# Performance work log

Hardware: AMD Instinct MI355X
Metric: run time of the kernel (lower is better)

Reference implementation:

```python
import jax, jax.numpy as jnp
import numpy as np

N_NODES, N_EDGES, N_TRIP = 100000, 200000, 600000
HID, HEADS, RADIUS = 256, 8, 3
ATOM_F, BOND_F = 133, 14

def setup_inputs() -> dict:
    key = jax.random.key(0)
    ks = jax.random.split(key, 20)
    def w(k, i, o):
        return jax.random.normal(k, (i, o), dtype=jnp.float32) / np.sqrt(i)
    L = RADIUS - 1
    return {
        'atom_feature': jax.random.normal(ks[0], (N_NODES, ATOM_F), dtype=jnp.float32),
        'edge_feature': jax.random.normal(ks[1], (N_EDGES, BOND_F), dtype=jnp.float32),
        'W_i': w(ks[2], ATOM_F + BOND_F, HID),
        'Wq': jnp.stack([w(jax.random.fold_in(ks[3], l), HID, HID) for l in range(L)]),
        'Wk': jnp.stack([w(jax.random.fold_in(ks[4], l), HID, HID) for l in range(L)]),
        'Wv': jnp.stack([w(jax.random.fold_in(ks[5], l), HID, HID) for l in range(L)]),
        'L1w': jnp.stack([w(jax.random.fold_in(ks[6], l), HID, HID) for l in range(L)]),
        'L1b': jnp.zeros((L, HID), dtype=jnp.float32),
        'L2w': jnp.stack([w(jax.random.fold_in(ks[7], l), HID, HID) for l in range(L)]),
        'L2b': jnp.zeros((L, HID), dtype=jnp.float32),
        'Wo': w(ks[8], ATOM_F + HID, HID),
        'bo': jnp.zeros((HID,), dtype=jnp.float32),
        'src': jax.random.randint(ks[9], (N_EDGES,), 0, N_NODES, dtype=jnp.int32),
        'dst': jax.random.randint(ks[10], (N_EDGES,), 0, N_NODES, dtype=jnp.int32),
        'idx_kj': jax.random.randint(ks[11], (N_TRIP,), 0, N_EDGES, dtype=jnp.int32),
        'idx_ji': jax.random.randint(ks[12], (N_TRIP,), 0, N_EDGES, dtype=jnp.int32),
    }

def _att_layer(feats, Wq, Wk, Wv, l1w, l1b, l2w, l2b, idx_kj, idx_ji):
    E = feats.shape[0]
    d = HID // HEADS
    q = (feats @ Wq).reshape(E, HEADS, d)
    k = (feats @ Wk).reshape(E, HEADS, d)
    v = (feats @ Wv).reshape(E, HEADS, d)
    # per-triplet attention logits [T, heads, 1]
    att = jnp.sum(q[idx_kj] * k[idx_ji], axis=-1, keepdims=True)
    att = jnp.exp(jax.nn.leaky_relu(att, negative_slope=0.2))
    denom = jax.ops.segment_sum(att, idx_ji, num_segments=E)  # edge softmax norm
    att = att / denom[idx_ji]
    v_att = (v[idx_kj] * att).reshape(-1, HID)
    v_flat = v.reshape(E, HID)
    # v_clone = v + index_add(v_att) - v == segment_sum of messages
    v_clone = jax.ops.segment_sum(v_att, idx_ji, num_segments=E)
    # residual MLP (dropout p=0 -> identity)
    h = jax.nn.relu(jax.nn.relu(v_clone @ l1w + l1b) @ l2w + l2b)
    return v_flat + h

def reference(atom_feature, edge_feature, W_i, Wq, Wk, Wv, L1w, L1b, L2w, L2b, Wo, bo, src, dst, idx_kj, idx_ji):
    # per-edge initial feature: concat(src atom feature, edge feature)
    init = jnp.concatenate([atom_feature[src], edge_feature], axis=1)
    feats = jax.nn.relu(init @ W_i)
    for l in range(RADIUS - 1):
        feats = _att_layer(feats, Wq[l], Wk[l], Wv[l], L1w[l], L1b[l], L2w[l], L2b[l], idx_kj, idx_ji)
    # edge -> node sum (dgl update_all copy_e + sum onto dst)
    feats_sum = jax.ops.segment_sum(feats, dst, num_segments=atom_feature.shape[0])
    a_input = jnp.concatenate([atom_feature, feats_sum], axis=1)
    return jax.nn.relu(a_input @ Wo + bo)
```

## Files before the change

kernel.cpp:

```cpp
#include <hip/hip_runtime.h>
#include <stdint.h>

#define NN 100000
#define NNP 100096
#define NE 200000
#define NEP 200064
#define NT 600000
#define HID 256

typedef __attribute__((ext_vector_type(8))) short bf16x8;
typedef __attribute__((ext_vector_type(4))) float f32x4;

__device__ __forceinline__ float bf2f(unsigned short u) {
    union { unsigned int i; float f; } x; x.i = ((unsigned int)u) << 16; return x.f;
}
__device__ __forceinline__ unsigned short f2bf(float f) {
    union { float f; unsigned int i; } x; x.f = f;
    unsigned int r = (x.i + 0x7FFFu + ((x.i >> 16) & 1u)) >> 16;
    return (unsigned short)r;
}

__device__ __forceinline__ void gload16(const void* g, void* l) {
    __builtin_amdgcn_global_load_lds(
        (const __attribute__((address_space(1))) void*)g,
        (__attribute__((address_space(3))) void*)l, 16, 0, 0);
}

template<int FLAGS, bool CBF>
__device__ __forceinline__
void gemm128_core(const unsigned short* __restrict__ A,
                  const unsigned short* __restrict__ BT,
                  const float* __restrict__ bias,
                  const unsigned short* __restrict__ res,
                  void* __restrict__ Cv, int row0, int col0,
                  int Mreal, int Kpad,
                  unsigned short* Asb, unsigned short* Bsb)
{
    const int t    = threadIdx.x;
    const int lane = t & 63;
    const int wv   = t >> 6;
    const int wr   = wv >> 1;
    const int wc   = wv & 1;
    const int l15  = lane & 15;
    const int lk   = lane >> 4;
    const int sub  = lane >> 3;
    const int schk = lane & 7;

    f32x4 acc[4][4];
#pragma unroll
    for (int i = 0; i < 4; ++i)
#pragma unroll
        for (int j = 0; j < 4; ++j) acc[i][j] = (f32x4){0.f, 0.f, 0.f, 0.f};

    const int nt = Kpad >> 6;
    for (int kt = 0; kt < nt; ++kt) {
        const int k0 = kt << 6;
#pragma unroll
        for (int j = 0; j < 4; ++j) {
            const int ii = wv * 4 + j;
            const int r  = ii * 8 + sub;
            const int cg = schk ^ (r & 7);
            gload16(A + (size_t)(row0 + r) * Kpad + k0 + cg * 8, Asb + ii * 512);
        }
#pragma unroll
        for (int j = 0; j < 4; ++j) {
            const int ii = wv * 4 + j;
            const int r  = ii * 8 + sub;
            const int cg = schk ^ (r & 7);
            gload16(BT + (size_t)(col0 + r) * Kpad + k0 + cg * 8, Bsb + ii * 512);
        }
        __syncthreads();
#pragma unroll
        for (int ks = 0; ks < 2; ++ks) {
            bf16x8 af[4], bfg[4];
#pragma unroll
            for (int mi = 0; mi < 4; ++mi) {
                const int r = wr * 64 + mi * 16 + l15;
                const int c = ks * 4 + lk;
                af[mi] = *(const bf16x8*)((const char*)Asb
                          + r * 128 + ((c ^ (r & 7)) << 4));
            }
#pragma unroll
            for (int ni = 0; ni < 4; ++ni) {
                const int r = wc * 64 + ni * 16 + l15;
                const int c = ks * 4 + lk;
                bfg[ni] = *(const bf16x8*)((const char*)Bsb
                           + r * 128 + ((c ^ (r & 7)) << 4));
            }
#pragma unroll
            for (int mi = 0; mi < 4; ++mi)
#pragma unroll
                for (int ni = 0; ni < 4; ++ni)
                    acc[mi][ni] = __builtin_amdgcn_mfma_f32_16x16x32_bf16(
                        af[mi], bfg[ni], acc[mi][ni], 0, 0, 0);
        }
        __syncthreads();
    }

#pragma unroll
    for (int mi = 0; mi < 4; ++mi) {
#pragma unroll
        for (int r = 0; r < 4; ++r) {
            const int row = row0 + wr * 64 + mi * 16 + lk * 4 + r;
            if (row >= Mreal) continue;
#pragma unroll
            for (int ni = 0; ni < 4; ++ni) {
                const int col = col0 + wc * 64 + ni * 16 + l15;
                float o = acc[mi][ni][r];
                if (FLAGS & 2) o += bias[col];
                if (FLAGS & 1) o = fmaxf(o, 0.f);
                if (FLAGS & 4) o += bf2f(res[(size_t)row * HID + col]);
                if (CBF) ((unsigned short*)Cv)[(size_t)row * HID + col] = f2bf(o);
                else     ((float*)Cv)[(size_t)row * HID + col] = o;
            }
        }
    }
}

template<int FLAGS, bool CBF>
__global__ __launch_bounds__(256, 4)
void gemm128(const unsigned short* __restrict__ A,
             const unsigned short* __restrict__ BT,
             const float* __restrict__ bias,
             const unsigned short* __restrict__ res,
             void* __restrict__ Cv, int Mtiles, int Mreal, int Kpad)
{
    __shared__ alignas(16) unsigned short Asb[128 * 64];
    __shared__ alignas(16) unsigned short Bsb[128 * 64];
    const int x   = blockIdx.x;
    const int xcd = x & 7;
    const int ii  = x >> 3;
    const int g   = (ii >> 1) * 8 + xcd;
    const int ch  = ii & 1;
    if (g >= Mtiles) return;
    gemm128_core<FLAGS, CBF>(A, BT, bias, res, Cv, g * 128, ch * 128,
                             Mreal, Kpad, Asb, Bsb);
}

__global__ __launch_bounds__(256, 4)
void gemm128_qkv(const unsigned short* __restrict__ A,
                 const unsigned short* __restrict__ BTq,
                 const unsigned short* __restrict__ BTk,
                 const unsigned short* __restrict__ BTv,
                 unsigned short* __restrict__ Cq,
                 unsigned short* __restrict__ Ck,
                 unsigned short* __restrict__ Cvp, int Mtiles)
{
    __shared__ alignas(16) unsigned short Asb[128 * 64];
    __shared__ alignas(16) unsigned short Bsb[128 * 64];
    const int x   = blockIdx.x;
    const int xcd = x & 7;
    const int ii  = x >> 3;
    const int g   = (ii / 6) * 8 + xcd;
    const int j   = ii % 6;
    if (g >= Mtiles) return;
    const int proj = j >> 1;
    const int ch   = j & 1;
    const unsigned short* BT = (proj == 0) ? BTq : (proj == 1) ? BTk : BTv;
    unsigned short*       C  = (proj == 0) ? Cq  : (proj == 1) ? Ck  : Cvp;
    gemm128_core<0, true>(A, BT, nullptr, nullptr, C, g * 128, ch * 128,
                          NE, 256, Asb, Bsb);
}

__global__ __launch_bounds__(256)
void wconv(const float* __restrict__ W, unsigned short* __restrict__ BT,
           int Kreal, int Kpad)
{
    const int idx = blockIdx.x * 256 + threadIdx.x;
    const int n = idx / Kpad, kp = idx - n * Kpad;
    float v = (kp < Kreal) ? W[(size_t)kp * HID + n] : 0.f;
    BT[idx] = f2bf(v);
}

__global__ __launch_bounds__(256)
void wconv10(const float* __restrict__ Wq, const float* __restrict__ Wk,
             const float* __restrict__ Wv, const float* __restrict__ L1w,
             const float* __restrict__ L2w, unsigned short* __restrict__ outbase)
{
    const int y = blockIdx.y;
    const int l = y / 5, which = y - l * 5;
    const float* src;
    switch (which) {
        case 0: src = Wq;  break;
        case 1: src = Wk;  break;
        case 2: src = Wv;  break;
        case 3: src = L1w; break;
        default: src = L2w; break;
    }
    src += (size_t)l * 65536;
    const int idx = blockIdx.x * 256 + threadIdx.x;
    const int n = idx >> 8, kp = idx & 255;
    outbase[(size_t)y * 65536 + idx] = f2bf(src[(size_t)kp * HID + n]);
}

__global__ __launch_bounds__(256)
void build_initA(const float* __restrict__ atom, const float* __restrict__ edge,
                 const int* __restrict__ src, unsigned short* __restrict__ out)
{
    const long total = (long)NE * 192;
    long idx = (long)blockIdx.x * blockDim.x + threadIdx.x;
    if (idx >= total) return;
    const int e = (int)(idx / 192);
    const int c = (int)(idx - (long)e * 192);
    float v = 0.f;
    if (c < 133)      v = atom[(size_t)src[e] * 133 + c];
    else if (c < 147) v = edge[(size_t)e * 14 + (c - 133)];
    out[idx] = f2bf(v);
}

__global__ __launch_bounds__(256)
void build_finalA(const float* __restrict__ atom, const float* __restrict__ fsum,
                  unsigned short* __restrict__ out)
{
    const long total = (long)NNP * 448;
    long idx = (long)blockIdx.x * blockDim.x + threadIdx.x;
    if (idx >= total) return;
    const int n = (int)(idx / 448);
    const int c = (int)(idx - (long)n * 448);
    float v = 0.f;
    if (n < NN) {
        if (c < 133)      v = atom[(size_t)n * 133 + c];
        else if (c < 389) v = fsum[(size_t)n * 256 + (c - 133)];
    }
    out[idx] = f2bf(v);
}

__global__ __launch_bounds__(256)
void count_keys(const int* __restrict__ key, int n, int nkeys, int* __restrict__ cnt)
{
    const int i = blockIdx.x * 256 + threadIdx.x;
    if (i < n) {
        const int kk = key[i];
        if ((unsigned)kk < (unsigned)nkeys) atomicAdd(&cnt[kk], 1);
    }
}

__global__ __launch_bounds__(256)
void fill_lists(const int* __restrict__ key, int n, int nkeys, int cap,
                int* __restrict__ cur, int* __restrict__ list)
{
    const int i = blockIdx.x * 256 + threadIdx.x;
    if (i < n) {
        const int kk = key[i];
        if ((unsigned)kk >= (unsigned)nkeys) return;
        const int pos = atomicAdd(&cur[kk], 1);
        if ((unsigned)pos < (unsigned)cap) list[pos] = i;
    }
}

__global__ __launch_bounds__(256)
void build_tripkj(const int* __restrict__ tlist, const int* __restrict__ idx_kj,
                  int* __restrict__ tkj)
{
    const int p = blockIdx.x * 256 + threadIdx.x;
    if (p >= NT) return;
    const int tt = tlist[p];
    int kj = -1;
    if ((unsigned)tt < (unsigned)NT) kj = idx_kj[tt];
    tkj[p] = kj;
}

__global__ __launch_bounds__(256)
void scan1(const int* __restrict__ in, int n, int* __restrict__ excl,
           int* __restrict__ part)
{
    __shared__ int sh[256];
    const int t = threadIdx.x;
    const int base = blockIdx.x * 1024 + t * 4;
    int v[4]; int s = 0;
#pragma unroll
    for (int j = 0; j < 4; ++j) { v[j] = (base + j < n) ? in[base + j] : 0; s += v[j]; }
    sh[t] = s; __syncthreads();
    for (int off = 1; off < 256; off <<= 1) {
        int x = (t >= off) ? sh[t - off] : 0;
        __syncthreads();
        sh[t] += x;
        __syncthreads();
    }
    int ex = sh[t] - s;
#pragma unroll
    for (int j = 0; j < 4; ++j) { if (base + j < n) excl[base + j] = ex; ex += v[j]; }
    if (t == 255) part[blockIdx.x] = sh[255];
}

__global__ __launch_bounds__(256)
void scan2(int* __restrict__ part, int nparts)
{
    __shared__ int sh[256];
    const int t = threadIdx.x;
    const int v = (t < nparts) ? part[t] : 0;
    sh[t] = v; __syncthreads();
    for (int off = 1; off < 256; off <<= 1) {
        int x = (t >= off) ? sh[t - off] : 0;
        __syncthreads();
        sh[t] += x;
        __syncthreads();
    }
    if (t < nparts) part[t] = sh[t] - v;
}

__global__ __launch_bounds__(256)
void scan3(const int* __restrict__ excl, const int* __restrict__ part,
           const int* counts, int n, int* __restrict__ offs, int* cur)
{
    const int i = blockIdx.x * 256 + threadIdx.x;
    if (i >= n) return;
    const int v = excl[i] + part[i >> 10];
    const int c = counts[i];
    offs[i] = v;
    cur[i] = v;
    if (i == n - 1) offs[n] = v + c;
}

__global__ __launch_bounds__(256)
void gather_v(const unsigned short* __restrict__ q, const unsigned short* __restrict__ k,
              const unsigned short* __restrict__ v,
              const int* __restrict__ toff, const int* __restrict__ tkj,
              unsigned short* __restrict__ vc)
{
    const long gtid = (long)blockIdx.x * blockDim.x + threadIdx.x;
    const int w    = (int)(gtid >> 5);
    const int lane = threadIdx.x & 31;
    if (w >= NE) return;
    int beg = toff[w], end = toff[w + 1];
    if (beg < 0) beg = 0;
    if (end > NT) end = NT;

    const bf16x8 kv = *(const bf16x8*)(k + (size_t)w * HID + lane * 8);
    float kf[8];
#pragma unroll
    for (int j = 0; j < 8; ++j) kf[j] = bf2f((unsigned short)kv[j]);

    float av[8];
#pragma unroll
    for (int j = 0; j < 8; ++j) av[j] = 0.f;
    float den = 0.f;

    int kj_next = (beg < end) ? tkj[beg] : -1;
    for (int p = beg; p < end; ++p) {
        const int kj = kj_next;
        if (p + 1 < end) kj_next = tkj[p + 1];
        if ((unsigned)kj >= (unsigned)NE) continue;
        const bf16x8 qv = *(const bf16x8*)(q + (size_t)kj * HID + lane * 8);
        float s = 0.f;
#pragma unroll
        for (int j = 0; j < 8; ++j) s += bf2f((unsigned short)qv[j]) * kf[j];
        s += __shfl_xor(s, 1);
        s += __shfl_xor(s, 2);
        const float lr = (s > 0.f) ? s : 0.2f * s;
        const float a  = __expf(lr);
        den += a;
        const bf16x8 vv = *(const bf16x8*)(v + (size_t)kj * HID + lane * 8);
#pragma unroll
        for (int j = 0; j < 8; ++j) av[j] += a * bf2f((unsigned short)vv[j]);
    }
    const float inv = (den != 0.f) ? 1.f / den : 0.f;
    bf16x8 o;
#pragma unroll
    for (int j = 0; j < 8; ++j) o[j] = (short)f2bf(av[j] * inv);
    *(bf16x8*)(vc + (size_t)w * HID + lane * 8) = o;
}

__global__ __launch_bounds__(256)
void gather_node(const unsigned short* __restrict__ feats,
                 const int* __restrict__ noff, const int* __restrict__ nlist,
                 float* __restrict__ fsum)
{
    const int w    = (int)(((long)blockIdx.x * blockDim.x + threadIdx.x) >> 6);
    const int lane = threadIdx.x & 63;
    if (w >= NN) return;
    int beg = noff[w], end = noff[w + 1];
    if (beg < 0) beg = 0;
    if (end > NE) end = NE;
    float a0 = 0.f, a1 = 0.f, a2 = 0.f, a3 = 0.f;
    for (int p = beg; p < end; ++p) {
        const int e = nlist[p];
        if ((unsigned)e >= (unsigned)NE) continue;
        const ushort4 f = *(const ushort4*)(feats + (size_t)e * HID + lane * 4);
        a0 += bf2f(f.x); a1 += bf2f(f.y); a2 += bf2f(f.z); a3 += bf2f(f.w);
    }
    float4 o = make_float4(a0, a1, a2, a3);
    *(float4*)(fsum + (size_t)w * HID + lane * 4) = o;
}

extern "C" void kernel_launch(void* const* d_in, const int* in_sizes, int n_in,
                              void* d_out, int out_size, void* d_ws, size_t ws_size,
                              hipStream_t stream)
{
    const float* atom = (const float*)d_in[0];
    const float* edge = (const float*)d_in[1];
    const float* W_i  = (const float*)d_in[2];
    const float* Wq   = (const float*)d_in[3];
    const float* Wk   = (const float*)d_in[4];
    const float* Wv   = (const float*)d_in[5];
    const float* L1w  = (const float*)d_in[6];
    const float* L1b  = (const float*)d_in[7];
    const float* L2w  = (const float*)d_in[8];
    const float* L2b  = (const float*)d_in[9];
    const float* Wo   = (const float*)d_in[10];
    const float* bo   = (const float*)d_in[11];
    const int* src    = (const int*)d_in[12];
    const int* dst    = (const int*)d_in[13];
    const int* idx_kj = (const int*)d_in[14];
    const int* idx_ji = (const int*)d_in[15];

    const size_t RB = (size_t)NE * HID * 2;
    char* ws = (char*)d_ws;
    unsigned short* feats = (unsigned short*)(ws);
    unsigned short* qb    = (unsigned short*)(ws + RB);
    unsigned short* kb    = (unsigned short*)(ws + 2 * RB);
    unsigned short* vb    = (unsigned short*)d_out;
    unsigned short* vc    = feats;
    unsigned short* initA = qb;
    unsigned short* h1    = kb;
    float*          fsum  = (float*)(ws + RB);
    unsigned short* finalA = kb;

    char* p = ws + 3 * RB;
    int* trip_off  = (int*)p; p += 800016;
    int* trip_cur  = (int*)p; p += 800016;
    int* trip_list = (int*)p; p += 2400000;
    int* trip_kj   = (int*)p; p += 2400000;
    int* node_off  = (int*)p; p += 400016;
    int* node_cur  = (int*)p; p += 400016;
    int* node_list = (int*)p; p += 800000;
    int* tmp_excl  = (int*)p; p += 800016;
    int* partials  = (int*)p; p += 1024;
    unsigned short* wiT = (unsigned short*)p; p += (size_t)256 * 192 * 2;
    unsigned short* wT0 = (unsigned short*)p; p += (size_t)10 * 65536 * 2;
    unsigned short* woT = (unsigned short*)p; p += (size_t)256 * 448 * 2;
    const size_t NEEDED = (size_t)(p - ws);
    if (ws_size < NEEDED) return;
    auto wT = [&](int i) { return wT0 + (size_t)i * 65536; };

    const int MT_E  = NEP / 128;
    const int MT_E8 = ((MT_E + 7) / 8) * 8;
    const int MT_N  = NNP / 128;
    const int MT_N8 = ((MT_N + 7) / 8) * 8;

    wconv<<<192, 256, 0, stream>>>(W_i, wiT, 147, 192);
    wconv10<<<dim3(256, 10), 256, 0, stream>>>(Wq, Wk, Wv, L1w, L2w, wT0);
    wconv<<<448, 256, 0, stream>>>(Wo, woT, 389, 448);

    hipMemsetAsync(trip_cur, 0, (size_t)NE * 4, stream);
    hipMemsetAsync(node_cur, 0, (size_t)NN * 4, stream);
    count_keys<<<(NT + 255) / 256, 256, 0, stream>>>(idx_ji, NT, NE, trip_cur);
    count_keys<<<(NE + 255) / 256, 256, 0, stream>>>(dst, NE, NN, node_cur);

    scan1<<<(NE + 1023) / 1024, 256, 0, stream>>>(trip_cur, NE, tmp_excl, partials);
    scan2<<<1, 256, 0, stream>>>(partials, (NE + 1023) / 1024);
    scan3<<<(NE + 255) / 256, 256, 0, stream>>>(tmp_excl, partials, trip_cur, NE, trip_off, trip_cur);
    fill_lists<<<(NT + 255) / 256, 256, 0, stream>>>(idx_ji, NT, NE, NT, trip_cur, trip_list);
    build_tripkj<<<(NT + 255) / 256, 256, 0, stream>>>(trip_list, idx_kj, trip_kj);

    scan1<<<(NN + 1023) / 1024, 256, 0, stream>>>(node_cur, NN, tmp_excl, partials);
    scan2<<<1, 256, 0, stream>>>(partials, (NN + 1023) / 1024);
    scan3<<<(NN + 255) / 256, 256, 0, stream>>>(tmp_excl, partials, node_cur, NN, node_off, node_cur);
    fill_lists<<<(NE + 255) / 256, 256, 0, stream>>>(dst, NE, NN, NE, node_cur, node_list);

    {
        const long total = (long)NE * 192;
        build_initA<<<(int)((total + 255) / 256), 256, 0, stream>>>(atom, edge, src, initA);
    }
    gemm128<1, true><<<MT_E8 * 2, 256, 0, stream>>>(initA, wiT, nullptr, nullptr,
                                                    feats, MT_E, NE, 192);

    for (int l = 0; l < 2; ++l) {
        const float* l1b = L1b + (size_t)l * 256;
        const float* l2b = L2b + (size_t)l * 256;

        gemm128_qkv<<<MT_E8 * 6, 256, 0, stream>>>(
            feats, wT(l * 5 + 0), wT(l * 5 + 1), wT(l * 5 + 2), qb, kb, vb, MT_E);

        gather_v<<<(NE * 32) / 256, 256, 0, stream>>>(qb, kb, vb, trip_off, trip_kj, vc);

        gemm128<3, true><<<MT_E8 * 2, 256, 0, stream>>>(vc, wT(l * 5 + 3), l1b,
                                                        nullptr, h1, MT_E, NE, 256);
        gemm128<7, true><<<MT_E8 * 2, 256, 0, stream>>>(h1, wT(l * 5 + 4), l2b,
                                                        vb, feats, MT_E, NE, 256);
    }

    gather_node<<<NN / 4, 256, 0, stream>>>(feats, node_off, node_list, fsum);
    {
        const long total = (long)NNP * 448;
        build_finalA<<<(int)((total + 255) / 256), 256, 0, stream>>>(atom, fsum, finalA);
    }
    gemm128<3, false><<<MT_N8 * 2, 256, 0, stream>>>(finalA, woT, bo, nullptr,
                                                     d_out, MT_N, NN, 448);
}
```

Measured before the change: 1.309 ms.

## Merge triplet and node CSR construction into one scan and fuse kj fill

Concatenates the edge-keyed triplet counts and node-keyed edge counts into one key array so a single memset and a single three-stage scan build both offset tables. The fill kernel now writes idx_kj directly into the triplet list, which removes the separate build_tripkj pass and its intermediate list. gather_node switches to 32 lanes per node with 16-byte loads and a prefetched next index. These steps are meant to cut kernel launches and setup passes, but setup is a small share of total time.

```diff
diff --git a/kernel.cpp b/kernel.cpp
--- a/kernel.cpp
+++ b/kernel.cpp
@@ -236,28 +236,27 @@
 }
 
 __global__ __launch_bounds__(256)
-void fill_lists(const int* __restrict__ key, int n, int nkeys, int cap,
-                int* __restrict__ cur, int* __restrict__ list)
+void fill_trip(const int* __restrict__ idx_ji, const int* __restrict__ idx_kj,
+               int* __restrict__ cur, int* __restrict__ plist)
 {
     const int i = blockIdx.x * 256 + threadIdx.x;
-    if (i < n) {
-        const int kk = key[i];
-        if ((unsigned)kk >= (unsigned)nkeys) return;
-        const int pos = atomicAdd(&cur[kk], 1);
-        if ((unsigned)pos < (unsigned)cap) list[pos] = i;
-    }
-}
-
-__global__ __launch_bounds__(256)
-void build_tripkj(const int* __restrict__ tlist, const int* __restrict__ idx_kj,
-                  int* __restrict__ tkj)
-{
-    const int p = blockIdx.x * 256 + threadIdx.x;
-    if (p >= NT) return;
-    const int tt = tlist[p];
-    int kj = -1;
-    if ((unsigned)tt < (unsigned)NT) kj = idx_kj[tt];
-    tkj[p] = kj;
+    if (i >= NT) return;
+    const int kk = idx_ji[i];
+    if ((unsigned)kk >= (unsigned)NE) return;
+    const int pos = atomicAdd(&cur[kk], 1);
+    if ((unsigned)pos < (unsigned)NT) plist[pos] = idx_kj[i];
+}
+
+__global__ __launch_bounds__(256)
+void fill_node(const int* __restrict__ dst, int* __restrict__ cur,
+               int* __restrict__ plist)
+{
+    const int i = blockIdx.x * 256 + threadIdx.x;
+    if (i >= NE) return;
+    const int kk = dst[i];
+    if ((unsigned)kk >= (unsigned)NN) return;
+    const int pos = atomicAdd(&cur[NE + kk], 1);
+    if ((unsigned)pos < (unsigned)(NT + NE)) plist[pos] = i;
 }
 
 __global__ __launch_bounds__(256)
@@ -266,10 +265,10 @@
 {
     __shared__ int sh[256];
     const int t = threadIdx.x;
-    const int base = blockIdx.x * 1024 + t * 4;
-    int v[4]; int s = 0;
-#pragma unroll
-    for (int j = 0; j < 4; ++j) { v[j] = (base + j < n) ? in[base + j] : 0; s += v[j]; }
+    const int base = blockIdx.x * 2048 + t * 8;
+    int v[8]; int s = 0;
+#pragma unroll
+    for (int j = 0; j < 8; ++j) { v[j] = (base + j < n) ? in[base + j] : 0; s += v[j]; }
     sh[t] = s; __syncthreads();
     for (int off = 1; off < 256; off <<= 1) {
         int x = (t >= off) ? sh[t - off] : 0;
@@ -279,7 +278,7 @@
     }
     int ex = sh[t] - s;
 #pragma unroll
-    for (int j = 0; j < 4; ++j) { if (base + j < n) excl[base + j] = ex; ex += v[j]; }
+    for (int j = 0; j < 8; ++j) { if (base + j < n) excl[base + j] = ex; ex += v[j]; }
     if (t == 255) part[blockIdx.x] = sh[255];
 }
 
@@ -305,7 +304,7 @@
 {
     const int i = blockIdx.x * 256 + threadIdx.x;
     if (i >= n) return;
-    const int v = excl[i] + part[i >> 10];
+    const int v = excl[i] + part[i >> 11];
     const int c = counts[i];
     offs[i] = v;
     cur[i] = v;
@@ -366,21 +365,30 @@
                  const int* __restrict__ noff, const int* __restrict__ nlist,
                  float* __restrict__ fsum)
 {
-    const int w    = (int)(((long)blockIdx.x * blockDim.x + threadIdx.x) >> 6);
-    const int lane = threadIdx.x & 63;
+    const long gtid = (long)blockIdx.x * blockDim.x + threadIdx.x;
+    const int w    = (int)(gtid >> 5);
+    const int lane = threadIdx.x & 31;
     if (w >= NN) return;
     int beg = noff[w], end = noff[w + 1];
     if (beg < 0) beg = 0;
-    if (end > NE) end = NE;
-    float a0 = 0.f, a1 = 0.f, a2 = 0.f, a3 = 0.f;
+    if (end > NT + NE) end = NT + NE;
+    float av[8];
+#pragma unroll
+    for (int j = 0; j < 8; ++j) av[j] = 0.f;
+    int e_next = (beg < end) ? nlist[beg] : -1;
     for (int p = beg; p < end; ++p) {
-        const int e = nlist[p];
+        const int e = e_next;
+        if (p + 1 < end) e_next = nlist[p + 1];
         if ((unsigned)e >= (unsigned)NE) continue;
-        const ushort4 f = *(const ushort4*)(feats + (size_t)e * HID + lane * 4);
-        a0 += bf2f(f.x); a1 += bf2f(f.y); a2 += bf2f(f.z); a3 += bf2f(f.w);
-    }
-    float4 o = make_float4(a0, a1, a2, a3);
-    *(float4*)(fsum + (size_t)w * HID + lane * 4) = o;
+        const bf16x8 f = *(const bf16x8*)(feats + (size_t)e * HID + lane * 8);
+#pragma unroll
+        for (int j = 0; j < 8; ++j) av[j] += bf2f((unsigned short)f[j]);
+    }
+    float4 o0 = make_float4(av[0], av[1], av[2], av[3]);
+    float4 o1 = make_float4(av[4], av[5], av[6], av[7]);
+    float* out = fsum + (size_t)w * HID + lane * 8;
+    *reinterpret_cast<float4*>(out)     = o0;
+    *reinterpret_cast<float4*>(out + 4) = o1;
 }
 
 extern "C" void kernel_launch(void* const* d_in, const int* in_sizes, int n_in,
@@ -416,16 +424,13 @@
     float*          fsum  = (float*)(ws + RB);
     unsigned short* finalA = kb;
 
+    const int NK = NE + NN;
     char* p = ws + 3 * RB;
-    int* trip_off  = (int*)p; p += 800016;
-    int* trip_cur  = (int*)p; p += 800016;
-    int* trip_list = (int*)p; p += 2400000;
-    int* trip_kj   = (int*)p; p += 2400000;
-    int* node_off  = (int*)p; p += 400016;
-    int* node_cur  = (int*)p; p += 400016;
-    int* node_list = (int*)p; p += 800000;
-    int* tmp_excl  = (int*)p; p += 800016;
-    int* partials  = (int*)p; p += 1024;
+    int* offs     = (int*)p; p += ((size_t)NK + 16) * 4;
+    int* cur      = (int*)p; p += ((size_t)NK + 16) * 4;
+    int* plist    = (int*)p; p += (size_t)(NT + NE) * 4;
+    int* tmp_excl = (int*)p; p += ((size_t)NK + 16) * 4;
+    int* partials = (int*)p; p += 1024;
     unsigned short* wiT = (unsigned short*)p; p += (size_t)256 * 192 * 2;
     unsigned short* wT0 = (unsigned short*)p; p += (size_t)10 * 65536 * 2;
     unsigned short* woT = (unsigned short*)p; p += (size_t)256 * 448 * 2;
@@ -437,26 +442,20 @@
     const int MT_E8 = ((MT_E + 7) / 8) * 8;
     const int MT_N  = NNP / 128;
     const int MT_N8 = ((MT_N + 7) / 8) * 8;
+    const int NPARTS = (NK + 2047) / 2048;
 
     wconv<<<192, 256, 0, stream>>>(W_i, wiT, 147, 192);
     wconv10<<<dim3(256, 10), 256, 0, stream>>>(Wq, Wk, Wv, L1w, L2w, wT0);
     wconv<<<448, 256, 0, stream>>>(Wo, woT, 389, 448);
 
-    hipMemsetAsync(trip_cur, 0, (size_t)NE * 4, stream);
-    hipMemsetAsync(node_cur, 0, (size_t)NN * 4, stream);
-    count_keys<<<(NT + 255) / 256, 256, 0, stream>>>(idx_ji, NT, NE, trip_cur);
-    count_keys<<<(NE + 255) / 256, 256, 0, stream>>>(dst, NE, NN, node_cur);
-
-    scan1<<<(NE + 1023) / 1024, 256, 0, stream>>>(trip_cur, NE, tmp_excl, partials);
-    scan2<<<1, 256, 0, stream>>>(partials, (NE + 1023) / 1024);
-    scan3<<<(NE + 255) / 256, 256, 0, stream>>>(tmp_excl, partials, trip_cur, NE, trip_off, trip_cur);
-    fill_lists<<<(NT + 255) / 256, 256, 0, stream>>>(idx_ji, NT, NE, NT, trip_cur, trip_list);
-    build_tripkj<<<(NT + 255) / 256, 256, 0, stream>>>(trip_list, idx_kj, trip_kj);
-
-    scan1<<<(NN + 1023) / 1024, 256, 0, stream>>>(node_cur, NN, tmp_excl, partials);
-    scan2<<<1, 256, 0, stream>>>(partials, (NN + 1023) / 1024);
-    scan3<<<(NN + 255) / 256, 256, 0, stream>>>(tmp_excl, partials, node_cur, NN, node_off, node_cur);
-    fill_lists<<<(NE + 255) / 256, 256, 0, stream>>>(dst, NE, NN, NE, node_cur, node_list);
+    hipMemsetAsync(cur, 0, (size_t)NK * 4, stream);
+    count_keys<<<(NT + 255) / 256, 256, 0, stream>>>(idx_ji, NT, NE, cur);
+    count_keys<<<(NE + 255) / 256, 256, 0, stream>>>(dst, NE, NN, cur + NE);
+    scan1<<<NPARTS, 256, 0, stream>>>(cur, NK, tmp_excl, partials);
+    scan2<<<1, 256, 0, stream>>>(partials, NPARTS);
+    scan3<<<(NK + 255) / 256, 256, 0, stream>>>(tmp_excl, partials, cur, NK, offs, cur);
+    fill_trip<<<(NT + 255) / 256, 256, 0, stream>>>(idx_ji, idx_kj, cur, plist);
+    fill_node<<<(NE + 255) / 256, 256, 0, stream>>>(dst, cur, plist);
 
     {
         const long total = (long)NE * 192;
@@ -472,7 +471,7 @@
         gemm128_qkv<<<MT_E8 * 6, 256, 0, stream>>>(
             feats, wT(l * 5 + 0), wT(l * 5 + 1), wT(l * 5 + 2), qb, kb, vb, MT_E);
 
-        gather_v<<<(NE * 32) / 256, 256, 0, stream>>>(qb, kb, vb, trip_off, trip_kj, vc);
+        gather_v<<<(NE * 32) / 256, 256, 0, stream>>>(qb, kb, vb, offs, plist, vc);
 
         gemm128<3, true><<<MT_E8 * 2, 256, 0, stream>>>(vc, wT(l * 5 + 3), l1b,
                                                         nullptr, h1, MT_E, NE, 256);
@@ -480,7 +479,7 @@
                                                         vb, feats, MT_E, NE, 256);
     }
 
-    gather_node<<<NN / 4, 256, 0, stream>>>(feats, node_off, node_list, fsum);
+    gather_node<<<(NN * 32) / 256, 256, 0, stream>>>(feats, offs + NE, plist, fsum);
     {
         const long total = (long)NNP * 448;
         build_finalA<<<(int)((total + 255) / 256), 256, 0, stream>>>(atom, fsum, finalA);
```

After: 1.278 ms. 1.02x faster.
